# Kernel optimization log

Hardware: AMD Instinct MI355X
Metric: run time of the kernel (lower is better)

Reference implementation:

```python
import jax, jax.numpy as jnp
import numpy as np

N, E, DIM = 20000, 500000, 2
KS = 5                 # kernel size per pseudo-dim (open spline)
K = KS ** DIM          # 25 kernel weight matrices (+1 root weight)
IN_F, OUT_F = 64, 64
S = 2 ** DIM           # support size of degree-1 B-spline basis


def setup_inputs() -> dict:
    key = jax.random.key(0)
    k1, k2, k3, k4, k5 = jax.random.split(key, 5)
    x = jax.random.normal(k1, (N, IN_F), jnp.float32)
    edge_index = jax.random.randint(k2, (2, E), 0, N)          # row=target, col=source
    pseudo = jax.random.uniform(k3, (E, DIM), jnp.float32)     # u(i,j) in [0,1]^dim
    weight = jax.random.normal(k4, (K + 1, IN_F, OUT_F), jnp.float32) * 0.05
    bias = jax.random.normal(k5, (OUT_F,), jnp.float32) * 0.05
    return {"x": x, "edge_index": edge_index, "pseudo": pseudo,
            "weight": weight, "bias": bias}


def _spline_basis(pseudo):
    """Degree-1 open B-spline tensor-product basis.
    Returns basis values [E,S] and flat kernel indices [E,S]."""
    u = pseudo * (KS - 1)                                      # [E,DIM]
    i0 = jnp.clip(jnp.floor(u).astype(jnp.int32), 0, KS - 2)   # lower knot per dim
    frac = u - i0.astype(u.dtype)                              # [E,DIM]
    bases, idxs = [], []
    for s in range(S):
        b = jnp.ones((pseudo.shape[0],), pseudo.dtype)
        idx = jnp.zeros((pseudo.shape[0],), jnp.int32)
        for d in range(DIM):
            bit = (s >> d) & 1
            w = frac[:, d] if bit else (1.0 - frac[:, d])
            b = b * w
            idx = idx * KS + (i0[:, d] + bit)                  # row-major flat index
        bases.append(b)
        idxs.append(idx)
    return jnp.stack(bases, 1), jnp.stack(idxs, 1)             # [E,S], [E,S]


def reference(x, edge_index, pseudo, weight, bias):
    row, col = edge_index[0], edge_index[1]
    basis, kidx = _spline_basis(pseudo)                        # [E,S]
    xj = x[col]                                                # gather neighbors [E,IN]
    # scatter B-spline-weighted neighbor features into (target node, kernel idx) buckets
    seg = (row[:, None].astype(jnp.int32) * K + kidx).reshape(-1)          # [E*S]
    vals = (basis[:, :, None] * xj[:, None, :]).reshape(-1, IN_F)          # [E*S,IN]
    agg = jax.ops.segment_sum(vals, seg, num_segments=N * K)
    agg = agg.reshape(N, K, IN_F)
    out = jnp.einsum('nki,kio->no', agg, weight[:K])           # basis-indexed matmuls
    deg = jax.ops.segment_sum(jnp.ones((E,), x.dtype), row, num_segments=N)
    out = out / jnp.clip(deg, 1.0)[:, None]                    # 1/|N(i)| normalization
    out = out + x @ weight[K] + bias                           # root weight + bias
    return out
```

## Files before the change

kernel.cpp:

```cpp
#include <hip/hip_runtime.h>
#include <hip/hip_bf16.h>
#include <cstdint>

constexpr int N_NODES = 20000;
constexpr int N_EDGES = 500000;
constexpr int IN_F    = 64;
constexpr int OUT_F   = 64;
constexpr int KS      = 5;
constexpr int K_MATS  = 25;
constexpr int NK      = 26;
constexpr int ZTILE_USH = 1024;

typedef __attribute__((ext_vector_type(8))) short short8;
typedef __attribute__((ext_vector_type(4))) float f32x4;

__device__ __forceinline__ ushort f2bf(float f) {
    union { float f; uint32_t u; } c; c.f = f;
    uint32_t u = c.u + 0x7FFFu + ((c.u >> 16) & 1u);
    return (ushort)(u >> 16);
}
__device__ __forceinline__ float bf2f(uint32_t s) {
    union { uint32_t u; float f; } c; c.u = (s & 0xFFFFu) << 16;
    return c.f;
}


constexpr int PREP_BLOCKS = (NK * 2 * 4 * 64) / 256;
constexpr int HIST_BLOCKS = (N_EDGES + 255) / 256;

__global__ void k_ph(const float* __restrict__ w, ushort* __restrict__ wb,
                     const int* __restrict__ ei, int* __restrict__ cnt) {
    int b = blockIdx.x;
    if (b < PREP_BLOCKS) {
        int t = b * 256 + threadIdx.x;
        int lane = t & 63;
        int nf   = (t >> 6) & 3;
        int ks   = (t >> 8) & 1;
        int k    = t >> 9;
        int kk0  = ks * 32 + (lane >> 4) * 8;
        int col  = nf * 16 + (lane & 15);
        ushort v[8];
#pragma unroll
        for (int j = 0; j < 8; ++j)
            v[j] = f2bf(w[(k * 64 + kk0 + j) * 64 + col]);
        uint4 p;
        p.x = (uint32_t)v[0] | ((uint32_t)v[1] << 16);
        p.y = (uint32_t)v[2] | ((uint32_t)v[3] << 16);
        p.z = (uint32_t)v[4] | ((uint32_t)v[5] << 16);
        p.w = (uint32_t)v[6] | ((uint32_t)v[7] << 16);
        ((uint4*)wb)[t] = p;
    } else {
        int e = (b - PREP_BLOCKS) * 256 + threadIdx.x;
        if (e < N_EDGES) atomicAdd(&cnt[ei[e]], 1);
    }
}

__global__ __launch_bounds__(1024) void k_scan(const int* __restrict__ cnt,
                                               int* __restrict__ row_start) {
    __shared__ int sums[1024];
    const int T = 1024;
    int tid = threadIdx.x;
    const int per = (N_NODES + T - 1) / T;
    int base = tid * per;
    int s = 0;
    for (int j = 0; j < per; ++j) {
        int idx = base + j;
        if (idx < N_NODES) s += cnt[idx];
    }
    sums[tid] = s;
    __syncthreads();
    for (int off = 1; off < T; off <<= 1) {
        int v = (tid >= off) ? sums[tid - off] : 0;
        __syncthreads();
        sums[tid] += v;
        __syncthreads();
    }
    int run = (tid == 0) ? 0 : sums[tid - 1];
    for (int j = 0; j < per; ++j) {
        int idx = base + j;
        if (idx < N_NODES) { row_start[idx] = run; run += cnt[idx]; }
    }
    if (tid == T - 1) row_start[N_NODES] = run;
}

__global__ void k_fill(const int* __restrict__ ei, const float* __restrict__ pseudo,
                       const int* __restrict__ row_start, int* __restrict__ fill_pos,
                       uint4* __restrict__ rec) {
    int e = blockIdx.x * blockDim.x + threadIdx.x;
    if (e >= N_EDGES) return;
    int row = ei[e];
    int col = ei[N_EDGES + e];
    float u0 = pseudo[2 * e]     * (float)(KS - 1);
    float u1 = pseudo[2 * e + 1] * (float)(KS - 1);
    int i0 = min(max((int)floorf(u0), 0), KS - 2);
    int i1 = min(max((int)floorf(u1), 0), KS - 2);
    float f0 = u0 - (float)i0;
    float f1 = u1 - (float)i1;
    float b00 = (1.f - f0) * (1.f - f1);
    float b10 = f0 * (1.f - f1);
    float b01 = (1.f - f0) * f1;
    float b11 = f0 * f1;
    int k00 = i0 * KS + i1;
    int k10 = (i0 + 1) * KS + i1;
    int pos = row_start[row] + atomicAdd(&fill_pos[row], 1);
    uint4 r;
    r.x = (uint32_t)col;
    r.y = (uint32_t)(k00 | (k10 << 8) | ((k00 + 1) << 16) | ((k10 + 1) << 24));
    r.z = (uint32_t)f2bf(b00) | ((uint32_t)f2bf(b10) << 16);
    r.w = (uint32_t)f2bf(b01) | ((uint32_t)f2bf(b11) << 16);
    rec[pos] = r;
}

constexpr int ZBLKS = N_NODES / 16;

__global__ __launch_bounds__(256) void k_z(const float* __restrict__ x,
                                           const ushort* __restrict__ wb,
                                           ushort* __restrict__ z) {
    __shared__ float lds[4][16][66];
    int lane = threadIdx.x & 63;
    int wave = threadIdx.x >> 6;
    int tile = blockIdx.x;
    int node0 = tile * 16;
    int r  = lane & 15;
    int kg = lane >> 4;

    short8 a[2];
#pragma unroll
    for (int ks = 0; ks < 2; ++ks) {
        const float4* xp = (const float4*)(x + (node0 + r) * IN_F + ks * 32 + kg * 8);
        float4 x0 = xp[0];
        float4 x1 = xp[1];
        short8 af;
        af[0] = (short)f2bf(x0.x); af[1] = (short)f2bf(x0.y);
        af[2] = (short)f2bf(x0.z); af[3] = (short)f2bf(x0.w);
        af[4] = (short)f2bf(x1.x); af[5] = (short)f2bf(x1.y);
        af[6] = (short)f2bf(x1.z); af[7] = (short)f2bf(x1.w);
        a[ks] = af;
    }

    for (int k = wave; k < NK; k += 4) {
        f32x4 acc[4];
#pragma unroll
        for (int nf = 0; nf < 4; ++nf) acc[nf] = (f32x4){0.f, 0.f, 0.f, 0.f};
#pragma unroll
        for (int ks = 0; ks < 2; ++ks) {
#pragma unroll
            for (int nf = 0; nf < 4; ++nf) {
                union { uint4 u; short8 s; } b;
                b.u = *(const uint4*)(wb + ((((size_t)k * 2 + ks) * 4 + nf) * 64 + lane) * 8);
                acc[nf] = __builtin_amdgcn_mfma_f32_16x16x32_bf16(a[ks], b.s, acc[nf], 0, 0, 0);
            }
        }
#pragma unroll
        for (int nf = 0; nf < 4; ++nf)
#pragma unroll
            for (int rg = 0; rg < 4; ++rg)
                lds[wave][kg * 4 + rg][nf * 16 + r] = acc[nf][rg];
        asm volatile("s_waitcnt lgkmcnt(0)" ::: "memory");
        __builtin_amdgcn_sched_barrier(0);
        const float* lrow = &lds[wave][lane >> 2][(lane & 3) * 16];
        float v[16];
#pragma unroll
        for (int j = 0; j < 16; ++j) v[j] = lrow[j];
        uint32_t pk[8];
#pragma unroll
        for (int j = 0; j < 8; ++j)
            pk[j] = (uint32_t)f2bf(v[2 * j]) | ((uint32_t)f2bf(v[2 * j + 1]) << 16);
        uint4* dst = (uint4*)(z + (size_t)(tile * NK + k) * ZTILE_USH + lane * 16);
        dst[0] = make_uint4(pk[0], pk[1], pk[2], pk[3]);
        dst[1] = make_uint4(pk[4], pk[5], pk[6], pk[7]);
        asm volatile("" ::: "memory");
    }
}

__global__ __launch_bounds__(256) void k_out(const ushort* __restrict__ z,
        const float* __restrict__ bias, const int* __restrict__ row_start,
        const uint4* __restrict__ rec, float* __restrict__ out) {
    int lane = threadIdx.x & 63;
    int n = blockIdx.x * 4 + (threadIdx.x >> 6);
    if (n >= N_NODES) return;
    int e0 = row_start[n], e1 = row_start[n + 1];
    float acc0 = 0.f, acc1 = 0.f;
    int e = e0;
    for (; e + 8 <= e1; e += 8) {
        uint4 rr[8];
#pragma unroll
        for (int t = 0; t < 8; ++t) rr[t] = rec[e + t];
        float vv[8][4];
#pragma unroll
        for (int t = 0; t < 8; ++t) {
            uint32_t kp = rr[t].y;
            uint32_t base = (rr[t].x >> 4) * (uint32_t)(NK * ZTILE_USH)
                          + (rr[t].x & 15) * 64u + (uint32_t)lane;
            vv[t][0] = bf2f((uint32_t)z[base + ((kp      ) & 255) * 1024u]);
            vv[t][1] = bf2f((uint32_t)z[base + ((kp >> 8 ) & 255) * 1024u]);
            vv[t][2] = bf2f((uint32_t)z[base + ((kp >> 16) & 255) * 1024u]);
            vv[t][3] = bf2f((uint32_t)z[base + ((kp >> 24)      ) * 1024u]);
        }
#pragma unroll
        for (int t = 0; t < 8; ++t) {
            float b0 = bf2f(rr[t].z), b1 = bf2f(rr[t].z >> 16);
            float b2 = bf2f(rr[t].w), b3 = bf2f(rr[t].w >> 16);
            float s = b0 * vv[t][0] + b1 * vv[t][1] + b2 * vv[t][2] + b3 * vv[t][3];
            if (t & 1) acc1 += s; else acc0 += s;
        }
    }
    for (; e + 4 <= e1; e += 4) {
        uint4 rr[4];
#pragma unroll
        for (int t = 0; t < 4; ++t) rr[t] = rec[e + t];
        float vv[4][4];
#pragma unroll
        for (int t = 0; t < 4; ++t) {
            uint32_t kp = rr[t].y;
            uint32_t base = (rr[t].x >> 4) * (uint32_t)(NK * ZTILE_USH)
                          + (rr[t].x & 15) * 64u + (uint32_t)lane;
            vv[t][0] = bf2f((uint32_t)z[base + ((kp      ) & 255) * 1024u]);
            vv[t][1] = bf2f((uint32_t)z[base + ((kp >> 8 ) & 255) * 1024u]);
            vv[t][2] = bf2f((uint32_t)z[base + ((kp >> 16) & 255) * 1024u]);
            vv[t][3] = bf2f((uint32_t)z[base + ((kp >> 24)      ) * 1024u]);
        }
#pragma unroll
        for (int t = 0; t < 4; ++t) {
            float b0 = bf2f(rr[t].z), b1 = bf2f(rr[t].z >> 16);
            float b2 = bf2f(rr[t].w), b3 = bf2f(rr[t].w >> 16);
            float s = b0 * vv[t][0] + b1 * vv[t][1] + b2 * vv[t][2] + b3 * vv[t][3];
            if (t & 1) acc1 += s; else acc0 += s;
        }
    }
    for (; e < e1; ++e) {
        uint4 r = rec[e];
        uint32_t kp = r.y;
        uint32_t base = (r.x >> 4) * (uint32_t)(NK * ZTILE_USH)
                      + (r.x & 15) * 64u + (uint32_t)lane;
        float v0 = bf2f((uint32_t)z[base + ((kp      ) & 255) * 1024u]);
        float v1 = bf2f((uint32_t)z[base + ((kp >> 8 ) & 255) * 1024u]);
        float v2 = bf2f((uint32_t)z[base + ((kp >> 16) & 255) * 1024u]);
        float v3 = bf2f((uint32_t)z[base + ((kp >> 24)      ) * 1024u]);
        acc0 += bf2f(r.z) * v0 + bf2f(r.z >> 16) * v1
              + bf2f(r.w) * v2 + bf2f(r.w >> 16) * v3;
    }
    int deg = e1 - e0;
    uint32_t rbase = ((uint32_t)(n >> 4) * NK + K_MATS) * (uint32_t)ZTILE_USH
                   + (uint32_t)(n & 15) * 64u + (uint32_t)lane;
    float root = bf2f((uint32_t)z[rbase]);
    out[n * OUT_F + lane] = (acc0 + acc1) / (float)max(deg, 1) + root + bias[lane];
}


extern "C" void kernel_launch(void* const* d_in, const int* in_sizes, int n_in,
                              void* d_out, int out_size, void* d_ws, size_t ws_size,
                              hipStream_t stream) {
    const float* x      = (const float*)d_in[0];
    const int*   ei     = (const int*)d_in[1];
    const float* pseudo = (const float*)d_in[2];
    const float* weight = (const float*)d_in[3];
    const float* bias   = (const float*)d_in[4];
    float* out = (float*)d_out;

    char* ws = (char*)d_ws;
    int* cnt       = (int*)(ws + 0);
    int* fill_pos  = (int*)(ws + 80000);
    int* row_start = (int*)(ws + 160000);
    uint4* rec     = (uint4*)(ws + 240128);
    ushort* wb     = (ushort*)(ws + 8240128);
    ushort* zb     = (ushort*)(ws + 8453120);

    hipMemsetAsync(ws, 0, 160000, stream);

    k_ph<<<PREP_BLOCKS + HIST_BLOCKS, 256, 0, stream>>>(weight, wb, ei, cnt);
    k_scan<<<1, 1024, 0, stream>>>(cnt, row_start);
    k_fill<<<HIST_BLOCKS, 256, 0, stream>>>(ei, pseudo, row_start, fill_pos, rec);
    k_z<<<ZBLKS, 256, 0, stream>>>(x, wb, zb);
    k_out<<<(N_NODES + 3) / 4, 256, 0, stream>>>(zb, bias, row_start, rec, out);
}
```

Baseline: 209.0 us.

## Fuse all stages into one cooperative persistent kernel with grid syncs

Replaces the five separate launches (prep/histogram, scan, fill, z transform, output gather) with a single cooperative kernel that uses grid-wide syncs between phases. The scan runs in block 0 while the remaining blocks compute the bf16 z transform, overlapping the serial scan with the MFMA work. It removes per-launch overhead and idle gaps between kernels. In exchange it adds grid barrier costs, limits the grid to resident blocks, and keeps the old multi-kernel path as a fallback if the cooperative launch fails.

Result: slower. 556.8 us (+166.3%).

```diff
diff --git a/kernel.cpp b/kernel.cpp
--- a/kernel.cpp
+++ b/kernel.cpp
@@ -1,6 +1,9 @@
 #include <hip/hip_runtime.h>
 #include <hip/hip_bf16.h>
+#include <hip/hip_cooperative_groups.h>
 #include <cstdint>
+
+namespace cg = cooperative_groups;
 
 constexpr int N_NODES = 20000;
 constexpr int N_EDGES = 500000;
@@ -10,6 +13,10 @@
 constexpr int K_MATS  = 25;
 constexpr int NK      = 26;
 constexpr int ZTILE_USH = 1024;
+constexpr int ZBLKS = N_NODES / 16;
+constexpr int PREP_ITEMS = NK * 2 * 4 * 64;
+constexpr int PREP_BLOCKS = PREP_ITEMS / 256;
+constexpr int HIST_BLOCKS = (N_EDGES + 255) / 256;
 
 typedef __attribute__((ext_vector_type(8))) short short8;
 typedef __attribute__((ext_vector_type(4))) float f32x4;
@@ -24,9 +31,229 @@
     return c.f;
 }
 
-
-constexpr int PREP_BLOCKS = (NK * 2 * 4 * 64) / 256;
-constexpr int HIST_BLOCKS = (N_EDGES + 255) / 256;
+__global__ __launch_bounds__(256) void k_mega(
+        const float* __restrict__ x, const int* __restrict__ ei,
+        const float* __restrict__ pseudo, const float* __restrict__ weight,
+        const float* __restrict__ bias, int* __restrict__ cnt,
+        int* __restrict__ fill_pos, int* __restrict__ row_start,
+        uint4* __restrict__ rec, ushort* __restrict__ wb,
+        ushort* __restrict__ z, float* __restrict__ out) {
+    cg::grid_group grid = cg::this_grid();
+    __shared__ float lds[4][16][66];
+    __shared__ int   sums[256];
+
+    const int gt = blockIdx.x * 256 + threadIdx.x;
+    const int gs = gridDim.x * 256;
+
+    for (int t = gt; t < PREP_ITEMS; t += gs) {
+        int lane = t & 63;
+        int nf   = (t >> 6) & 3;
+        int ks   = (t >> 8) & 1;
+        int k    = t >> 9;
+        int kk0  = ks * 32 + (lane >> 4) * 8;
+        int col  = nf * 16 + (lane & 15);
+        ushort v[8];
+#pragma unroll
+        for (int j = 0; j < 8; ++j)
+            v[j] = f2bf(weight[(k * 64 + kk0 + j) * 64 + col]);
+        uint4 p;
+        p.x = (uint32_t)v[0] | ((uint32_t)v[1] << 16);
+        p.y = (uint32_t)v[2] | ((uint32_t)v[3] << 16);
+        p.z = (uint32_t)v[4] | ((uint32_t)v[5] << 16);
+        p.w = (uint32_t)v[6] | ((uint32_t)v[7] << 16);
+        ((uint4*)wb)[t] = p;
+    }
+    for (int e = gt; e < N_EDGES; e += gs)
+        atomicAdd(&cnt[ei[e]], 1);
+    __threadfence();
+    grid.sync();
+
+    if (blockIdx.x == 0) {
+        const int T = 256;
+        int tid = threadIdx.x;
+        const int per = (N_NODES + T - 1) / T;
+        int base = tid * per;
+        int s = 0;
+        for (int j = 0; j < per; ++j) {
+            int idx = base + j;
+            if (idx < N_NODES) s += cnt[idx];
+        }
+        sums[tid] = s;
+        __syncthreads();
+        for (int off = 1; off < T; off <<= 1) {
+            int v = (tid >= off) ? sums[tid - off] : 0;
+            __syncthreads();
+            sums[tid] += v;
+            __syncthreads();
+        }
+        int run = (tid == 0) ? 0 : sums[tid - 1];
+        for (int j = 0; j < per; ++j) {
+            int idx = base + j;
+            if (idx < N_NODES) { row_start[idx] = run; run += cnt[idx]; }
+        }
+        if (tid == T - 1) row_start[N_NODES] = run;
+    }
+    if (blockIdx.x != 0 || gridDim.x == 1) {
+        int tstart = (gridDim.x == 1) ? 0 : (int)blockIdx.x - 1;
+        int tstride = (gridDim.x == 1) ? 1 : (int)gridDim.x - 1;
+        int lane = threadIdx.x & 63;
+        int wave = threadIdx.x >> 6;
+        int r  = lane & 15;
+        int kg = lane >> 4;
+        for (int tile = tstart; tile < ZBLKS; tile += tstride) {
+            int node0 = tile * 16;
+            short8 a[2];
+#pragma unroll
+            for (int ks = 0; ks < 2; ++ks) {
+                const float4* xp = (const float4*)(x + (node0 + r) * IN_F + ks * 32 + kg * 8);
+                float4 x0 = xp[0];
+                float4 x1 = xp[1];
+                short8 af;
+                af[0] = (short)f2bf(x0.x); af[1] = (short)f2bf(x0.y);
+                af[2] = (short)f2bf(x0.z); af[3] = (short)f2bf(x0.w);
+                af[4] = (short)f2bf(x1.x); af[5] = (short)f2bf(x1.y);
+                af[6] = (short)f2bf(x1.z); af[7] = (short)f2bf(x1.w);
+                a[ks] = af;
+            }
+            for (int k = wave; k < NK; k += 4) {
+                f32x4 acc[4];
+#pragma unroll
+                for (int nf = 0; nf < 4; ++nf) acc[nf] = (f32x4){0.f, 0.f, 0.f, 0.f};
+#pragma unroll
+                for (int ks = 0; ks < 2; ++ks) {
+#pragma unroll
+                    for (int nf = 0; nf < 4; ++nf) {
+                        union { uint4 u; short8 s; } b;
+                        b.u = *(const uint4*)(wb + ((((size_t)k * 2 + ks) * 4 + nf) * 64 + lane) * 8);
+                        acc[nf] = __builtin_amdgcn_mfma_f32_16x16x32_bf16(a[ks], b.s, acc[nf], 0, 0, 0);
+                    }
+                }
+#pragma unroll
+                for (int nf = 0; nf < 4; ++nf)
+#pragma unroll
+                    for (int rg = 0; rg < 4; ++rg)
+                        lds[wave][kg * 4 + rg][nf * 16 + r] = acc[nf][rg];
+                asm volatile("s_waitcnt lgkmcnt(0)" ::: "memory");
+                __builtin_amdgcn_sched_barrier(0);
+                const float* lrow = &lds[wave][lane >> 2][(lane & 3) * 16];
+                float v[16];
+#pragma unroll
+                for (int j = 0; j < 16; ++j) v[j] = lrow[j];
+                uint32_t pk[8];
+#pragma unroll
+                for (int j = 0; j < 8; ++j)
+                    pk[j] = (uint32_t)f2bf(v[2 * j]) | ((uint32_t)f2bf(v[2 * j + 1]) << 16);
+                uint4* dst = (uint4*)(z + (size_t)(tile * NK + k) * ZTILE_USH + lane * 16);
+                dst[0] = make_uint4(pk[0], pk[1], pk[2], pk[3]);
+                dst[1] = make_uint4(pk[4], pk[5], pk[6], pk[7]);
+                asm volatile("" ::: "memory");
+            }
+        }
+    }
+    __threadfence();
+    grid.sync();
+
+    for (int e = gt; e < N_EDGES; e += gs) {
+        int row = ei[e];
+        int col = ei[N_EDGES + e];
+        float u0 = pseudo[2 * e]     * (float)(KS - 1);
+        float u1 = pseudo[2 * e + 1] * (float)(KS - 1);
+        int i0 = min(max((int)floorf(u0), 0), KS - 2);
+        int i1 = min(max((int)floorf(u1), 0), KS - 2);
+        float f0 = u0 - (float)i0;
+        float f1 = u1 - (float)i1;
+        float b00 = (1.f - f0) * (1.f - f1);
+        float b10 = f0 * (1.f - f1);
+        float b01 = (1.f - f0) * f1;
+        float b11 = f0 * f1;
+        int k00 = i0 * KS + i1;
+        int k10 = (i0 + 1) * KS + i1;
+        int pos = row_start[row] + atomicAdd(&fill_pos[row], 1);
+        uint4 rr;
+        rr.x = (uint32_t)col;
+        rr.y = (uint32_t)(k00 | (k10 << 8) | ((k00 + 1) << 16) | ((k10 + 1) << 24));
+        rr.z = (uint32_t)f2bf(b00) | ((uint32_t)f2bf(b10) << 16);
+        rr.w = (uint32_t)f2bf(b01) | ((uint32_t)f2bf(b11) << 16);
+        rec[pos] = rr;
+    }
+    __threadfence();
+    grid.sync();
+
+    {
+        int lane = threadIdx.x & 63;
+        int wid = blockIdx.x * 4 + (threadIdx.x >> 6);
+        int wstride = gridDim.x * 4;
+        for (int n = wid; n < N_NODES; n += wstride) {
+            int e0 = row_start[n], e1 = row_start[n + 1];
+            float acc0 = 0.f, acc1 = 0.f;
+            int e = e0;
+            for (; e + 8 <= e1; e += 8) {
+                uint4 rr[8];
+#pragma unroll
+                for (int t = 0; t < 8; ++t) rr[t] = rec[e + t];
+                float vv[8][4];
+#pragma unroll
+                for (int t = 0; t < 8; ++t) {
+                    uint32_t kp = rr[t].y;
+                    uint32_t base = (rr[t].x >> 4) * (uint32_t)(NK * ZTILE_USH)
+                                  + (rr[t].x & 15) * 64u + (uint32_t)lane;
+                    vv[t][0] = bf2f((uint32_t)z[base + ((kp      ) & 255) * 1024u]);
+                    vv[t][1] = bf2f((uint32_t)z[base + ((kp >> 8 ) & 255) * 1024u]);
+                    vv[t][2] = bf2f((uint32_t)z[base + ((kp >> 16) & 255) * 1024u]);
+                    vv[t][3] = bf2f((uint32_t)z[base + ((kp >> 24)      ) * 1024u]);
+                }
+#pragma unroll
+                for (int t = 0; t < 8; ++t) {
+                    float b0 = bf2f(rr[t].z), b1 = bf2f(rr[t].z >> 16);
+                    float b2 = bf2f(rr[t].w), b3 = bf2f(rr[t].w >> 16);
+                    float s = b0 * vv[t][0] + b1 * vv[t][1] + b2 * vv[t][2] + b3 * vv[t][3];
+                    if (t & 1) acc1 += s; else acc0 += s;
+                }
+            }
+            for (; e + 4 <= e1; e += 4) {
+                uint4 rr[4];
+#pragma unroll
+                for (int t = 0; t < 4; ++t) rr[t] = rec[e + t];
+                float vv[4][4];
+#pragma unroll
+                for (int t = 0; t < 4; ++t) {
+                    uint32_t kp = rr[t].y;
+                    uint32_t base = (rr[t].x >> 4) * (uint32_t)(NK * ZTILE_USH)
+                                  + (rr[t].x & 15) * 64u + (uint32_t)lane;
+                    vv[t][0] = bf2f((uint32_t)z[base + ((kp      ) & 255) * 1024u]);
+                    vv[t][1] = bf2f((uint32_t)z[base + ((kp >> 8 ) & 255) * 1024u]);
+                    vv[t][2] = bf2f((uint32_t)z[base + ((kp >> 16) & 255) * 1024u]);
+                    vv[t][3] = bf2f((uint32_t)z[base + ((kp >> 24)      ) * 1024u]);
+                }
+#pragma unroll
+                for (int t = 0; t < 4; ++t) {
+                    float b0 = bf2f(rr[t].z), b1 = bf2f(rr[t].z >> 16);
+                    float b2 = bf2f(rr[t].w), b3 = bf2f(rr[t].w >> 16);
+                    float s = b0 * vv[t][0] + b1 * vv[t][1] + b2 * vv[t][2] + b3 * vv[t][3];
+                    if (t & 1) acc1 += s; else acc0 += s;
+                }
+            }
+            for (; e < e1; ++e) {
+                uint4 r = rec[e];
+                uint32_t kp = r.y;
+                uint32_t base = (r.x >> 4) * (uint32_t)(NK * ZTILE_USH)
+                              + (r.x & 15) * 64u + (uint32_t)lane;
+                float v0 = bf2f((uint32_t)z[base + ((kp      ) & 255) * 1024u]);
+                float v1 = bf2f((uint32_t)z[base + ((kp >> 8 ) & 255) * 1024u]);
+                float v2 = bf2f((uint32_t)z[base + ((kp >> 16) & 255) * 1024u]);
+                float v3 = bf2f((uint32_t)z[base + ((kp >> 24)      ) * 1024u]);
+                acc0 += bf2f(r.z) * v0 + bf2f(r.z >> 16) * v1
+                      + bf2f(r.w) * v2 + bf2f(r.w >> 16) * v3;
+            }
+            int deg = e1 - e0;
+            uint32_t rbase = ((uint32_t)(n >> 4) * NK + K_MATS) * (uint32_t)ZTILE_USH
+                           + (uint32_t)(n & 15) * 64u + (uint32_t)lane;
+            float root = bf2f((uint32_t)z[rbase]);
+            out[n * OUT_F + lane] = (acc0 + acc1) / (float)max(deg, 1) + root + bias[lane];
+        }
+    }
+}
+
 
 __global__ void k_ph(const float* __restrict__ w, ushort* __restrict__ wb,
                      const int* __restrict__ ei, int* __restrict__ cnt) {
@@ -111,8 +338,6 @@
     rec[pos] = r;
 }
 
-constexpr int ZBLKS = N_NODES / 16;
-
 __global__ __launch_bounds__(256) void k_z(const float* __restrict__ x,
                                            const ushort* __restrict__ wb,
                                            ushort* __restrict__ z) {
@@ -268,9 +493,22 @@
 
     hipMemsetAsync(ws, 0, 160000, stream);
 
-    k_ph<<<PREP_BLOCKS + HIST_BLOCKS, 256, 0, stream>>>(weight, wb, ei, cnt);
-    k_scan<<<1, 1024, 0, stream>>>(cnt, row_start);
-    k_fill<<<HIST_BLOCKS, 256, 0, stream>>>(ei, pseudo, row_start, fill_pos, rec);
-    k_z<<<ZBLKS, 256, 0, stream>>>(x, wb, zb);
-    k_out<<<(N_NODES + 3) / 4, 256, 0, stream>>>(zb, bias, row_start, rec, out);
-}
+    int nb = 0;
+    hipError_t oerr = hipOccupancyMaxActiveBlocksPerMultiprocessor(&nb, k_mega, 256, 0);
+    if (oerr != hipSuccess || nb < 1) nb = 2;
+    int grid = nb * 256;
+    if (grid < 2) grid = 2;
+
+    void* args[] = { (void*)&x, (void*)&ei, (void*)&pseudo, (void*)&weight,
+                     (void*)&bias, (void*)&cnt, (void*)&fill_pos, (void*)&row_start,
+                     (void*)&rec, (void*)&wb, (void*)&zb, (void*)&out };
+    hipError_t lerr = hipLaunchCooperativeKernel((const void*)k_mega, dim3(grid),
+                                                 dim3(256), args, 0, stream);
+    if (lerr != hipSuccess) {
+        k_ph<<<PREP_BLOCKS + HIST_BLOCKS, 256, 0, stream>>>(weight, wb, ei, cnt);
+        k_scan<<<1, 1024, 0, stream>>>(cnt, row_start);
+        k_fill<<<HIST_BLOCKS, 256, 0, stream>>>(ei, pseudo, row_start, fill_pos, rec);
+        k_z<<<ZBLKS, 256, 0, stream>>>(x, wb, zb);
+        k_out<<<(N_NODES + 3) / 4, 256, 0, stream>>>(zb, bias, row_start, rec, out);
+    }
+}
```
